# Optimization experiments

Hardware: AMD Instinct MI355X
Metric: run time of the kernel (lower is better)

Reference implementation:

```python
import jax, jax.numpy as jnp
import numpy as np

BETA = 0.25


def setup_inputs() -> dict:
    key = jax.random.key(0)
    k1, k2 = jax.random.split(key)
    inputs = jax.random.normal(k1, (32, 4096, 64), dtype=jnp.float32)
    # VarianceScaling(uniform) ~ small-magnitude init; plain normal scaled works for a numeric reference
    codebook = jax.random.normal(k2, (1024, 64), dtype=jnp.float32) * (1.0 / np.sqrt(64.0))
    return {"inputs": inputs, "codebook": codebook}


def reference(inputs, codebook):
    D = codebook.shape[-1]
    flat = jnp.reshape(inputs, (-1, D))                      # [N, D]
    flat_sqr = jnp.sum(flat ** 2, axis=-1, keepdims=True)    # [N, 1]
    code_sqr = jnp.sum(codebook ** 2, axis=-1)[None, :]      # [1, K]
    # full pairwise squared distances [N, K]
    distances = flat_sqr - 2.0 * (flat @ codebook.T) + code_sqr
    encoding_indices = jnp.reshape(jnp.argmin(distances, axis=-1), inputs.shape[:-1])
    quantize = codebook[encoding_indices]                    # gather -> [..., D]
    encoding_loss = jnp.mean((jax.lax.stop_gradient(inputs) - quantize) ** 2)
    commit_loss = jnp.mean((inputs - jax.lax.stop_gradient(quantize)) ** 2)
    loss = encoding_loss + BETA * commit_loss
    # straight-through estimator
    z_q = inputs + jax.lax.stop_gradient(quantize - inputs)
    return loss, z_q, encoding_indices
```

## Files before the change

### kernel.cpp

```cpp
#include <hip/hip_runtime.h>

#define N_ROWS 131072
#define D 64
#define K_CODES 1024
#define NTILE 64

typedef _Float16 f16x8 __attribute__((ext_vector_type(8)));
typedef float    f32x4 __attribute__((ext_vector_type(4)));

#define MFMA16(a, b, c) __builtin_amdgcn_mfma_f32_16x16x32_f16((a), (b), (c), 0, 0, 0)

__global__ __launch_bounds__(256)
void prep_kernel(const float* __restrict__ CB, _Float16* __restrict__ CBf,
                 float* __restrict__ csqr, float* __restrict__ loss) {
    const int b = blockIdx.x, t = threadIdx.x;
    if (b < 64) {
        const int unit = b * 256 + t;
        const int tile = unit >> 8;
        const int f    = (unit >> 6) & 3;
        const int lane = unit & 63;
        const int quad = lane >> 4, lrow = lane & 15;
        const int code = tile * 16 + lrow;
        const int k0   = (f & 1) * 32 + quad * 8;
        const float* src = CB + (size_t)code * D + k0;
        float4 v0 = *(const float4*)(src);
        float4 v1 = *(const float4*)(src + 4);
        float xs[8] = {v0.x, v0.y, v0.z, v0.w, v1.x, v1.y, v1.z, v1.w};
        f16x8 o;
#pragma unroll
        for (int j = 0; j < 8; ++j) {
            _Float16 h = (_Float16)xs[j];
            o[j] = (f < 2) ? h : (_Float16)(xs[j] - (float)h);
        }
        *(f16x8*)(CBf + (size_t)unit * 8) = o;
    } else {
        if (t == 0) *loss = 0.0f;
        for (int k = t; k < K_CODES; k += 256) {
            const float4* p = (const float4*)(CB + (size_t)k * D);
            float s = 0.0f;
#pragma unroll
            for (int i = 0; i < 16; ++i) {
                float4 v = p[i];
                s += v.x * v.x + v.y * v.y + v.z * v.z + v.w * v.w;
            }
            csqr[k] = s;
        }
    }
}

__global__ __launch_bounds__(256, 3)
void argmin_kernel(const float* __restrict__ X,
                   const _Float16* __restrict__ CBf,
                   const float* __restrict__ csqr,
                   const float* __restrict__ CB,
                   float* __restrict__ out) {
    __shared__ float LsC[K_CODES];

    const int t    = threadIdx.x;
    const int wave = t >> 6;
    const int lane = t & 63;
    const int lrow = lane & 15;
    const int quad = lane >> 4;
    const int R0   = blockIdx.x * 256 + wave * 64;

    float* const zq   = out + 1;
    float* const idxf = out + 1 + (size_t)N_ROWS * D;

    ((float4*)LsC)[t] = ((const float4*)csqr)[t];

    f16x8 Ah[4][2], Al[4][2];
    float xsq = 0.0f;
#pragma unroll
    for (int mt = 0; mt < 4; ++mt) {
        const float* xr = X + (size_t)(R0 + mt * 16 + lrow) * D;
#pragma unroll
        for (int ks = 0; ks < 2; ++ks) {
            const int k0 = ks * 32 + quad * 8;
            float4 v0 = *(const float4*)(xr + k0);
            float4 v1 = *(const float4*)(xr + k0 + 4);
            float xs[8] = {v0.x, v0.y, v0.z, v0.w, v1.x, v1.y, v1.z, v1.w};
            f16x8 h, l;
#pragma unroll
            for (int j = 0; j < 8; ++j) {
                xsq += xs[j] * xs[j];
                float sv = -2.0f * xs[j];
                _Float16 hh = (_Float16)sv;
                h[j] = hh;
                l[j] = (_Float16)(sv - (float)hh);
            }
            Ah[mt][ks] = h;
            Al[mt][ks] = l;
        }
    }
    __syncthreads();

    float bestd[4][4];
    int   besti[4][4];
#pragma unroll
    for (int mt = 0; mt < 4; ++mt)
#pragma unroll
        for (int r = 0; r < 4; ++r) { bestd[mt][r] = 3.0e38f; besti[mt][r] = 0; }

    const f16x8* gw = (const f16x8*)CBf + lane;

#define LOADB(Bv, tl)                                                         \
    do {                                                                      \
        const f16x8* _p = gw + (tl) * 256;                                    \
        Bv[0] = _p[0]; Bv[1] = _p[64]; Bv[2] = _p[128]; Bv[3] = _p[192];      \
    } while (0)

#define COMPUTE(Bv, tl)                                                       \
    do {                                                                      \
        const float cs = LsC[(tl) * 16 + lrow];                               \
        const int   c  = (tl) * 16 + lrow;                                    \
        _Pragma("unroll")                                                     \
        for (int mt = 0; mt < 4; ++mt) {                                      \
            f32x4 acc = {cs, cs, cs, cs};                                     \
            acc = MFMA16(Ah[mt][0], Bv[0], acc);                              \
            acc = MFMA16(Ah[mt][1], Bv[1], acc);                              \
            acc = MFMA16(Al[mt][0], Bv[0], acc);                              \
            acc = MFMA16(Al[mt][1], Bv[1], acc);                              \
            acc = MFMA16(Ah[mt][0], Bv[2], acc);                              \
            acc = MFMA16(Ah[mt][1], Bv[3], acc);                              \
            _Pragma("unroll")                                                 \
            for (int r = 0; r < 4; ++r) {                                     \
                bool lt = acc[r] < bestd[mt][r];                              \
                bestd[mt][r] = lt ? acc[r] : bestd[mt][r];                    \
                besti[mt][r] = lt ? c : besti[mt][r];                         \
            }                                                                 \
        }                                                                     \
    } while (0)

    f16x8 Ba[4], Bb[4];
    LOADB(Ba, 0);
    for (int tile = 0; tile < NTILE; tile += 2) {
        LOADB(Bb, tile + 1);
        COMPUTE(Ba, tile);
        LOADB(Ba, tile + 2);
        COMPUTE(Bb, tile + 1);
    }

    const float scale = 1.25f / (float)((size_t)N_ROWS * D);

#pragma unroll
    for (int m = 1; m < 64; m <<= 1) xsq += __shfl_xor(xsq, m, 64);

    float ssum = 0.0f;
#pragma unroll
    for (int mt = 0; mt < 4; ++mt) {
#pragma unroll
        for (int r = 0; r < 4; ++r) {
            float dv = bestd[mt][r];
            int   iv = besti[mt][r];
#pragma unroll
            for (int m = 1; m < 16; m <<= 1) {
                float od = __shfl_xor(dv, m, 64);
                int   oi = __shfl_xor(iv, m, 64);
                if (od < dv || (od == dv && oi < iv)) { dv = od; iv = oi; }
            }
            const int    row = R0 + mt * 16 + quad * 4 + r;
            const float* cr  = CB + (size_t)iv * D;
            float*       zr  = zq + (size_t)row * D;
            if (lrow < 15) {
                const int e = 3 + 4 * lrow;
                float4 cv = make_float4(cr[e], cr[e + 1], cr[e + 2], cr[e + 3]);
                *(float4*)(zr + e) = cv;
            } else {
                zr[0]  = cr[0];
                zr[1]  = cr[1];
                zr[2]  = cr[2];
                zr[63] = cr[63];
            }
            if (lrow == 0) {
                idxf[row] = (float)iv;
                ssum += dv;
            }
        }
    }
    ssum += __shfl_xor(ssum, 16, 64);
    ssum += __shfl_xor(ssum, 32, 64);
    if (lane == 0) atomicAdd(out, (xsq + ssum) * scale);
}

extern "C" void kernel_launch(void* const* d_in, const int* in_sizes, int n_in,
                              void* d_out, int out_size, void* d_ws,
                              size_t ws_size, hipStream_t stream) {
    const float* X  = (const float*)d_in[0];
    const float* CB = (const float*)d_in[1];

    float*    csqr = (float*)d_ws;
    _Float16* CBf  = (_Float16*)((char*)d_ws + 4096);

    hipLaunchKernelGGL(prep_kernel, dim3(65), dim3(256), 0, stream,
                       CB, CBf, csqr, (float*)d_out);
    hipLaunchKernelGGL(argmin_kernel, dim3(N_ROWS / 256), dim3(256), 0, stream,
                       X, CBf, csqr, CB, (float*)d_out);
}
```

Measured before the change: 165.6 us.

## Split codebook across waves per block and merge argmin candidates in shared memory

Each block now handles 64 rows instead of 256. Its four waves are arranged as 2 row-halves by 2 codebook-halves, so each wave keeps fewer A fragments and accumulators, and launch bounds rise to 4 blocks per SM. The per-half argmin candidates are merged through shared memory, and the block then writes the contiguous z_q region with coalesced float4 stores. The cost is extra syncthreads and shared traffic, and each wave reloads the codebook over 4x more blocks, which raises total B-fragment load traffic.

```diff
diff --git a/kernel.cpp b/kernel.cpp
--- a/kernel.cpp
+++ b/kernel.cpp
@@ -3,7 +3,6 @@
 #define N_ROWS 131072
 #define D 64
 #define K_CODES 1024
-#define NTILE 64
 
 typedef _Float16 f16x8 __attribute__((ext_vector_type(8)));
 typedef float    f32x4 __attribute__((ext_vector_type(4)));
@@ -48,31 +47,35 @@
     }
 }
 
-__global__ __launch_bounds__(256, 3)
+__global__ __launch_bounds__(256, 4)
 void argmin_kernel(const float* __restrict__ X,
                    const _Float16* __restrict__ CBf,
                    const float* __restrict__ csqr,
                    const float* __restrict__ CB,
                    float* __restrict__ out) {
     __shared__ float LsC[K_CODES];
+    __shared__ float candD[64][2];
+    __shared__ int   candI[64][2];
+    __shared__ int   ivfin[64];
+    __shared__ float xsqW[2];
 
     const int t    = threadIdx.x;
     const int wave = t >> 6;
     const int lane = t & 63;
     const int lrow = lane & 15;
     const int quad = lane >> 4;
-    const int R0   = blockIdx.x * 256 + wave * 64;
-
-    float* const zq   = out + 1;
-    float* const idxf = out + 1 + (size_t)N_ROWS * D;
+    const int rh   = wave >> 1;
+    const int ch   = wave & 1;
+    const int R0   = blockIdx.x * 64;
+    const int Rw   = R0 + rh * 32;
 
     ((float4*)LsC)[t] = ((const float4*)csqr)[t];
 
-    f16x8 Ah[4][2], Al[4][2];
+    f16x8 Ah[2][2], Al[2][2];
     float xsq = 0.0f;
 #pragma unroll
-    for (int mt = 0; mt < 4; ++mt) {
-        const float* xr = X + (size_t)(R0 + mt * 16 + lrow) * D;
+    for (int mt = 0; mt < 2; ++mt) {
+        const float* xr = X + (size_t)(Rw + mt * 16 + lrow) * D;
 #pragma unroll
         for (int ks = 0; ks < 2; ++ks) {
             const int k0 = ks * 32 + quad * 8;
@@ -94,14 +97,14 @@
     }
     __syncthreads();
 
-    float bestd[4][4];
-    int   besti[4][4];
-#pragma unroll
-    for (int mt = 0; mt < 4; ++mt)
+    float bestd[2][4];
+    int   besti[2][4];
+#pragma unroll
+    for (int mt = 0; mt < 2; ++mt)
 #pragma unroll
         for (int r = 0; r < 4; ++r) { bestd[mt][r] = 3.0e38f; besti[mt][r] = 0; }
 
-    const f16x8* gw = (const f16x8*)CBf + lane;
+    const f16x8* gw = (const f16x8*)CBf + (size_t)ch * 32 * 256 + lane;
 
 #define LOADB(Bv, tl)                                                         \
     do {                                                                      \
@@ -111,10 +114,10 @@
 
 #define COMPUTE(Bv, tl)                                                       \
     do {                                                                      \
-        const float cs = LsC[(tl) * 16 + lrow];                               \
-        const int   c  = (tl) * 16 + lrow;                                    \
+        const int   c  = (ch * 32 + (tl)) * 16 + lrow;                        \
+        const float cs = LsC[c];                                              \
         _Pragma("unroll")                                                     \
-        for (int mt = 0; mt < 4; ++mt) {                                      \
+        for (int mt = 0; mt < 2; ++mt) {                                      \
             f32x4 acc = {cs, cs, cs, cs};                                     \
             acc = MFMA16(Ah[mt][0], Bv[0], acc);                              \
             acc = MFMA16(Ah[mt][1], Bv[1], acc);                              \
@@ -133,21 +136,22 @@
 
     f16x8 Ba[4], Bb[4];
     LOADB(Ba, 0);
-    for (int tile = 0; tile < NTILE; tile += 2) {
-        LOADB(Bb, tile + 1);
-        COMPUTE(Ba, tile);
-        LOADB(Ba, tile + 2);
-        COMPUTE(Bb, tile + 1);
-    }
-
-    const float scale = 1.25f / (float)((size_t)N_ROWS * D);
-
-#pragma unroll
-    for (int m = 1; m < 64; m <<= 1) xsq += __shfl_xor(xsq, m, 64);
-
-    float ssum = 0.0f;
-#pragma unroll
-    for (int mt = 0; mt < 4; ++mt) {
+    for (int tl = 0; tl < 32; tl += 2) {
+        LOADB(Bb, tl + 1);
+        COMPUTE(Ba, tl);
+        LOADB(Ba, tl + 2);
+        COMPUTE(Bb, tl + 1);
+    }
+
+    if (ch == 0) {
+        float s = xsq;
+#pragma unroll
+        for (int m = 1; m < 64; m <<= 1) s += __shfl_xor(s, m, 64);
+        if (lane == 0) xsqW[rh] = s;
+    }
+
+#pragma unroll
+    for (int mt = 0; mt < 2; ++mt) {
 #pragma unroll
         for (int r = 0; r < 4; ++r) {
             float dv = bestd[mt][r];
@@ -158,28 +162,55 @@
                 int   oi = __shfl_xor(iv, m, 64);
                 if (od < dv || (od == dv && oi < iv)) { dv = od; iv = oi; }
             }
-            const int    row = R0 + mt * 16 + quad * 4 + r;
-            const float* cr  = CB + (size_t)iv * D;
-            float*       zr  = zq + (size_t)row * D;
-            if (lrow < 15) {
-                const int e = 3 + 4 * lrow;
-                float4 cv = make_float4(cr[e], cr[e + 1], cr[e + 2], cr[e + 3]);
-                *(float4*)(zr + e) = cv;
-            } else {
-                zr[0]  = cr[0];
-                zr[1]  = cr[1];
-                zr[2]  = cr[2];
-                zr[63] = cr[63];
-            }
             if (lrow == 0) {
-                idxf[row] = (float)iv;
-                ssum += dv;
-            }
-        }
-    }
-    ssum += __shfl_xor(ssum, 16, 64);
-    ssum += __shfl_xor(ssum, 32, 64);
-    if (lane == 0) atomicAdd(out, (xsq + ssum) * scale);
+                int rl = rh * 32 + mt * 16 + quad * 4 + r;
+                candD[rl][ch] = dv;
+                candI[rl][ch] = iv;
+            }
+        }
+    }
+    __syncthreads();
+
+    const float scale = 1.25f / (float)((size_t)N_ROWS * D);
+    if (t < 64) {
+        float d0 = candD[t][0], d1 = candD[t][1];
+        int   i0 = candI[t][0], i1 = candI[t][1];
+        bool take1 = d1 < d0;
+        float dv = take1 ? d1 : d0;
+        int   iv = take1 ? i1 : i0;
+        out[1 + (size_t)N_ROWS * D + R0 + t] = (float)iv;
+        ivfin[t] = iv;
+        float ssum = dv;
+#pragma unroll
+        for (int m = 1; m < 64; m <<= 1) ssum += __shfl_xor(ssum, m, 64);
+        if (t == 0)
+            atomicAdd(out, (ssum + xsqW[0] + xsqW[1]) * scale);
+    }
+    __syncthreads();
+
+    float* p = out + 1 + (size_t)R0 * D;
+#pragma unroll
+    for (int i = 0; i < 4; ++i) {
+        int q = i * 256 + t;
+        int j = 4 * q + 3;
+        if (q < 1023) {
+            float v[4];
+#pragma unroll
+            for (int e = 0; e < 4; ++e) {
+                int jj = j + e;
+                v[e] = CB[(size_t)ivfin[jj >> 6] * D + (jj & 63)];
+            }
+            *(float4*)(p + j) = make_float4(v[0], v[1], v[2], v[3]);
+        } else if (q == 1023) {
+            p[4095] = CB[(size_t)ivfin[63] * D + 63];
+        }
+    }
+    if (t == 0) {
+        const float* c0 = CB + (size_t)ivfin[0] * D;
+        p[0] = c0[0];
+        p[1] = c0[1];
+        p[2] = c0[2];
+    }
 }
 
 extern "C" void kernel_launch(void* const* d_in, const int* in_sizes, int n_in,
@@ -193,6 +224,6 @@
 
     hipLaunchKernelGGL(prep_kernel, dim3(65), dim3(256), 0, stream,
                        CB, CBf, csqr, (float*)d_out);
-    hipLaunchKernelGGL(argmin_kernel, dim3(N_ROWS / 256), dim3(256), 0, stream,
+    hipLaunchKernelGGL(argmin_kernel, dim3(N_ROWS / 64), dim3(256), 0, stream,
                        X, CBf, csqr, CB, (float*)d_out);
 }
```

Result: slower. 170.7 us (+3.1%).
